# Kernel tuning notes

Hardware: AMD Instinct MI355X
Metric: run time of the kernel (lower is better)

Reference implementation:

```python
import jax, jax.numpy as jnp
import numpy as np

B, C, D, H, W = 1, 64, 24, 24, 24
N = D * H * W
K = D + H + W - 2  # cross neighbors per node (self deduped)
DS, GD = 64, 64    # d_sim, g_dim
GROUPS = C // 4
EPS = 1e-5
N_ITERS = 2        # pool_strides = [1, 1]


def _build_nbr_idx():
    i, j, k = np.meshgrid(np.arange(D), np.arange(H), np.arange(W), indexing='ij')
    i, j, k = i.reshape(-1), j.reshape(-1), k.reshape(-1)
    a0 = (j * W + k)[:, None] + np.arange(D)[None, :] * (H * W)      # (N, D) full depth line (incl self)
    full1 = (i * H * W + k)[:, None] + np.arange(H)[None, :] * W     # (N, H)
    a1 = full1[np.arange(H)[None, :] != j[:, None]].reshape(N, H - 1)
    full2 = (i * H * W + j * W)[:, None] + np.arange(W)[None, :]     # (N, W)
    a2 = full2[np.arange(W)[None, :] != k[:, None]].reshape(N, W - 1)
    return np.concatenate([a0, a1, a2], axis=1).astype(np.int32)     # (N, K)


def setup_inputs() -> dict:
    key = jax.random.key(0)
    ks = jax.random.split(key, 8)
    s = 0.05
    return {
        'x': jax.random.normal(ks[0], (B, C, D, H, W), jnp.float32),
        'nbr_idx': jnp.asarray(_build_nbr_idx()),
        'phi_w': jax.random.normal(ks[1], (DS, C), jnp.float32) * s,
        'phi_b': jnp.zeros((DS,), jnp.float32),
        'theta_w': jax.random.normal(ks[2], (DS, C), jnp.float32) * s,
        'theta_b': jnp.zeros((DS,), jnp.float32),
        'G_w': jax.random.normal(ks[3], (GD, C), jnp.float32) * s,
        'G_b': jnp.zeros((GD,), jnp.float32),
        'r_w': jax.random.normal(ks[4], (C, GD), jnp.float32) * s,
        'r_b': jnp.zeros((C,), jnp.float32),
        'gn_gamma': jnp.ones((N_ITERS, C), jnp.float32),
        'gn_beta': jnp.zeros((N_ITERS, C), jnp.float32),
        'bn_gamma': jnp.ones((C,), jnp.float32),
        'bn_beta': jnp.zeros((C,), jnp.float32),
        'bn_mean': jnp.zeros((C,), jnp.float32),
        'bn_var': jnp.ones((C,), jnp.float32),
    }


def _group_norm(v, gamma, beta):
    vg = v.reshape(B, GROUPS, C // GROUPS, D, H, W)
    m = vg.mean(axis=(2, 3, 4, 5), keepdims=True)
    var = ((vg - m) ** 2).mean(axis=(2, 3, 4, 5), keepdims=True)
    vn = ((vg - m) / jnp.sqrt(var + EPS)).reshape(B, C, D, H, W)
    return vn * gamma[None, :, None, None, None] + beta[None, :, None, None, None]


def reference(x, nbr_idx, phi_w, phi_b, theta_w, theta_b, G_w, G_b, r_w, r_b,
              gn_gamma, gn_beta, bn_gamma, bn_beta, bn_mean, bn_var):
    h = x
    for it in range(N_ITERS):
        hf = h.reshape(B, C, N).transpose(2, 0, 1)                    # (N, B, C) node features
        theta = jnp.einsum('nbc,dc->nbd', hf, theta_w) + theta_b     # (N, B, DS) queries
        phi_all = jnp.einsum('nbc,dc->nbd', hf, phi_w) + phi_b       # (N, B, DS) keys (pre-gather)
        g_all = jnp.einsum('nbc,gc->nbg', hf, G_w) + G_b             # (N, B, GD) values (pre-gather)
        phi_e = phi_all[nbr_idx]                                      # (N, K, B, DS) mailbox gather
        g_e = g_all[nbr_idx]                                          # (N, K, B, GD)
        f = jnp.einsum('nbd,nkbd->nbk', theta, phi_e)                # attention logits over K
        a = jax.nn.softmax(f, axis=-1)                                # non_local_merge 'softmax'
        y = jnp.einsum('nbk,nkbg->nbg', a, g_e)                      # weighted value sum
        cross = jnp.einsum('nbg,cg->nbc', y, r_w) + r_b              # (N, B, C) output proj
        cross = cross.transpose(1, 2, 0).reshape(B, C, D, H, W)
        h = h + _group_norm(cross, gn_gamma[it], gn_beta[it])
    # BatchNorm3d (eval, running stats) + ReLU
    bc = lambda v: v[None, :, None, None, None]
    out = (h - bc(bn_mean)) / jnp.sqrt(bc(bn_var) + EPS) * bc(bn_gamma) + bc(bn_beta)
    return jax.nn.relu(out)
```

## Files before the change

kernel.cpp:

```cpp
#include <hip/hip_runtime.h>
#include <math.h>

#define NN 13824
#define LW 24

__global__ __launch_bounds__(256) void apply_proj_kernel(
    const float* __restrict__ x,
    const float* __restrict__ cross, const float* __restrict__ gsum,
    const float* __restrict__ gn_g, const float* __restrict__ gn_b,
    float* __restrict__ h_out, int mode,
    const float* __restrict__ theta_w, const float* __restrict__ theta_b,
    const float* __restrict__ phi_w, const float* __restrict__ phi_b,
    const float* __restrict__ g_w, const float* __restrict__ g_b,
    float* __restrict__ theta, float* __restrict__ phi, float* __restrict__ gv)
{
    __shared__ float hs[64 * 64];
    __shared__ float ws[64 * 68];

    const int tid = threadIdx.x;
    const int tile = blockIdx.x / 3, ts = blockIdx.x % 3;
    const int n0 = tile * 64;

    const float* wsel = (ts == 0) ? theta_w : (ts == 1) ? phi_w : g_w;
    const float* bsel = (ts == 0) ? theta_b : (ts == 1) ? phi_b : g_b;
    float*       osel = (ts == 0) ? theta   : (ts == 1) ? phi   : gv;

    if (mode == 0) {
        for (int i = tid; i < 4096; i += 256) {
            int c = i >> 6, nl = i & 63;
            hs[c * 64 + nl] = x[(size_t)c * NN + n0 + nl];
        }
    } else {
        for (int i = tid; i < 4096; i += 256) {
            int nl = i >> 6, c = i & 63;
            ws[c * 68 + nl] = cross[(size_t)(n0 + nl) * 64 + c];
        }
        __syncthreads();
        const float inv_cnt = 1.f / 55296.f;
        for (int i = tid; i < 4096; i += 256) {
            int c = i >> 6, nl = i & 63;
            int gr = c >> 2;
            float mean = gsum[gr * 16] * inv_cnt;
            float var = gsum[512 + gr * 16] * inv_cnt - mean * mean;
            float v = (ws[c * 68 + nl] - mean) * rsqrtf(var + 1e-5f) * gn_g[c] + gn_b[c];
            size_t o = (size_t)c * NN + n0 + nl;
            float hv = x[o] + v;
            hs[c * 64 + nl] = hv;
            if (ts == 0) h_out[o] = hv;
        }
        __syncthreads();
    }

    for (int i = tid; i < 4096; i += 256) {
        int d = i >> 6, c = i & 63;
        ws[c * 68 + d] = wsel[d * 64 + c];
    }
    __syncthreads();

    const int d0  = (tid & 15) * 4;
    const int nl0 = (tid >> 4) * 4;
    float acc[4][4];
    #pragma unroll
    for (int q = 0; q < 4; q++)
        #pragma unroll
        for (int j = 0; j < 4; j++) acc[q][j] = 0.f;

    #pragma unroll 4
    for (int c = 0; c < 64; c++) {
        float4 hv = *(const float4*)&hs[c * 64 + nl0];
        float4 wv = *(const float4*)&ws[c * 68 + d0];
        #pragma unroll
        for (int j = 0; j < 4; j++) {
            float w = (&wv.x)[j];
            acc[0][j] += hv.x * w;
            acc[1][j] += hv.y * w;
            acc[2][j] += hv.z * w;
            acc[3][j] += hv.w * w;
        }
    }
    float4 bias = *(const float4*)&bsel[d0];
    #pragma unroll
    for (int q = 0; q < 4; q++) {
        float4 v;
        v.x = acc[q][0] + bias.x; v.y = acc[q][1] + bias.y;
        v.z = acc[q][2] + bias.z; v.w = acc[q][3] + bias.w;
        *(float4*)&osel[(size_t)(n0 + nl0 + q) * 64 + d0] = v;
    }
}

__global__ __launch_bounds__(128) void line_attn_kernel(
    const float* __restrict__ theta,
    const float* __restrict__ phi,
    const float* __restrict__ gv,
    float* __restrict__ y_part,
    float* __restrict__ l_part,
    float* __restrict__ gsum)
{
    __shared__ float th[2][LW * 68], ph[2][LW * 68], gs[2][LW * 68];
    __shared__ float P[2][LW * 28];

    const int tid = threadIdx.x;
    const int wv = tid >> 6, lane = tid & 63;
    const int gl = blockIdx.x * 2 + wv;
    const int axis = gl / 576, L = gl % 576;

    if (blockIdx.x == 0) {
        for (int i = tid; i < 1024; i += 128) gsum[i] = 0.f;
    }

    int base, stride;
    if (axis == 0)      { base = L * 24;                    stride = 1;   }
    else if (axis == 1) { base = (L / 24) * 576 + (L % 24); stride = 24;  }
    else                { base = L;                         stride = 576; }
    const bool excl = (axis != 2);

    #pragma unroll
    for (int q = 0; q < 6; q++) {
        int idx = q * 64 + lane;
        int row = idx >> 4, c4 = (idx & 15) * 4;
        size_t g = (size_t)(base + row * stride) * 64 + c4;
        int la = row * 68 + c4;
        *(float4*)&th[wv][la] = *(const float4*)&theta[g];
        *(float4*)&ph[wv][la] = *(const float4*)&phi[g];
        *(float4*)&gs[wv][la] = *(const float4*)&gv[g];
    }

    const int r0 = (lane >> 3) * 3, c0 = (lane & 7) * 3;
    float sa[3][3];
    #pragma unroll
    for (int a = 0; a < 3; a++)
        #pragma unroll
        for (int b = 0; b < 3; b++) sa[a][b] = 0.f;

    #pragma unroll 4
    for (int d4 = 0; d4 < 64; d4 += 4) {
        float4 t[3], p[3];
        #pragma unroll
        for (int a = 0; a < 3; a++) t[a] = *(const float4*)&th[wv][(r0 + a) * 68 + d4];
        #pragma unroll
        for (int b = 0; b < 3; b++) p[b] = *(const float4*)&ph[wv][(c0 + b) * 68 + d4];
        #pragma unroll
        for (int a = 0; a < 3; a++)
            #pragma unroll
            for (int b = 0; b < 3; b++)
                sa[a][b] += t[a].x * p[b].x + t[a].y * p[b].y +
                            t[a].z * p[b].z + t[a].w * p[b].w;
    }
    #pragma unroll
    for (int a = 0; a < 3; a++)
        #pragma unroll
        for (int b = 0; b < 3; b++) {
            float e = (excl && (r0 + a) == (c0 + b)) ? 0.f : __expf(sa[a][b]);
            P[wv][(r0 + a) * 28 + c0 + b] = e;
        }

    if (lane < 24) {
        float s = 0.f;
        #pragma unroll
        for (int c4 = 0; c4 < 24; c4 += 4) {
            float4 pv = *(const float4*)&P[wv][lane * 28 + c4];
            s += pv.x + pv.y + pv.z + pv.w;
        }
        l_part[(size_t)axis * NN + base + lane * stride] = s;
    }

    float acc[24];
    #pragma unroll
    for (int r = 0; r < 24; r++) acc[r] = 0.f;
    #pragma unroll
    for (int c4 = 0; c4 < 24; c4 += 4) {
        float g0 = gs[wv][(c4 + 0) * 68 + lane];
        float g1 = gs[wv][(c4 + 1) * 68 + lane];
        float g2 = gs[wv][(c4 + 2) * 68 + lane];
        float g3 = gs[wv][(c4 + 3) * 68 + lane];
        #pragma unroll
        for (int r = 0; r < 24; r++) {
            float4 pv = *(const float4*)&P[wv][r * 28 + c4];
            acc[r] += pv.x * g0 + pv.y * g1 + pv.z * g2 + pv.w * g3;
        }
    }
    float* yp = y_part + (size_t)axis * NN * 64;
    #pragma unroll
    for (int r = 0; r < 24; r++)
        yp[(size_t)(base + r * stride) * 64 + lane] = acc[r];
}

__global__ __launch_bounds__(256) void combine_kernel(
    const float* __restrict__ y_part, const float* __restrict__ l_part,
    const float* __restrict__ r_w, const float* __restrict__ r_b,
    float* __restrict__ cross, float* __restrict__ gsum)
{
    __shared__ float ys[16 * 68];
    __shared__ float red_s[4][64], red_ss[4][64];

    const int tid = threadIdx.x;
    const int d = tid & 63, w = tid >> 6;
    const int n0 = blockIdx.x * 16;
    const size_t S = (size_t)NN * 64;

    #pragma unroll
    for (int q = 0; q < 4; q++) {
        int nn = w * 4 + q;
        int n = n0 + nn;
        float lv = l_part[n] + l_part[NN + n] + l_part[2 * NN + n];
        size_t o = (size_t)n * 64 + d;
        float yv = y_part[o] + y_part[S + o] + y_part[2 * S + o];
        ys[nn * 68 + d] = yv / lv;
    }
    __syncthreads();

    const int c = d;
    float rb = r_b[c];
    float acc[4] = {rb, rb, rb, rb};
    for (int dd = 0; dd < 64; dd += 4) {
        float4 r4 = *(const float4*)&r_w[c * 64 + dd];
        #pragma unroll
        for (int q = 0; q < 4; q++) {
            float4 y4 = *(const float4*)&ys[(w * 4 + q) * 68 + dd];
            acc[q] += r4.x * y4.x + r4.y * y4.y + r4.z * y4.z + r4.w * y4.w;
        }
    }
    float s = 0.f, ss = 0.f;
    #pragma unroll
    for (int q = 0; q < 4; q++) {
        int n = n0 + w * 4 + q;
        cross[(size_t)n * 64 + c] = acc[q];
        s += acc[q];
        ss += acc[q] * acc[q];
    }
    red_s[w][c] = s;
    red_ss[w][c] = ss;
    __syncthreads();
    if (w == 0) {
        float ts  = red_s[0][c] + red_s[1][c] + red_s[2][c] + red_s[3][c];
        float tss = red_ss[0][c] + red_ss[1][c] + red_ss[2][c] + red_ss[3][c];
        ts  += __shfl_xor(ts, 1);  ts  += __shfl_xor(ts, 2);
        tss += __shfl_xor(tss, 1); tss += __shfl_xor(tss, 2);
        if ((c & 3) == 0) {
            atomicAdd(&gsum[(c >> 2) * 16], ts);
            atomicAdd(&gsum[512 + (c >> 2) * 16], tss);
        }
    }
}

__global__ __launch_bounds__(256) void final_kernel(
    const float* __restrict__ cross,
    const float* __restrict__ gsum,
    const float* __restrict__ gn_g, const float* __restrict__ gn_b,
    const float* __restrict__ h_in,
    const float* __restrict__ bn_g, const float* __restrict__ bn_b,
    const float* __restrict__ bn_m, const float* __restrict__ bn_v,
    float* __restrict__ out)
{
    __shared__ float t[64 * 65];
    const int tid = threadIdx.x;
    const int n0 = blockIdx.x * 64;
    for (int i = tid; i < 4096; i += 256) {
        int nl = i >> 6, c = i & 63;
        t[c * 65 + nl] = cross[(size_t)(n0 + nl) * 64 + c];
    }
    __syncthreads();
    const float inv_cnt = 1.f / 55296.f;
    for (int i = tid; i < 4096; i += 256) {
        int c = i >> 6, nl = i & 63;
        int gr = c >> 2;
        float mean = gsum[gr * 16] * inv_cnt;
        float var = gsum[512 + gr * 16] * inv_cnt - mean * mean;
        float v = (t[c * 65 + nl] - mean) * rsqrtf(var + 1e-5f) * gn_g[c] + gn_b[c];
        size_t o = (size_t)c * NN + n0 + nl;
        float h2 = h_in[o] + v;
        float bnv = (h2 - bn_m[c]) * rsqrtf(bn_v[c] + 1e-5f) * bn_g[c] + bn_b[c];
        out[o] = fmaxf(bnv, 0.f);
    }
}

extern "C" void kernel_launch(void* const* d_in, const int* in_sizes, int n_in,
                              void* d_out, int out_size, void* d_ws, size_t ws_size,
                              hipStream_t stream)
{
    const float* x        = (const float*)d_in[0];
    const float* phi_w    = (const float*)d_in[2];
    const float* phi_b    = (const float*)d_in[3];
    const float* theta_w  = (const float*)d_in[4];
    const float* theta_b  = (const float*)d_in[5];
    const float* G_w      = (const float*)d_in[6];
    const float* G_b      = (const float*)d_in[7];
    const float* r_w      = (const float*)d_in[8];
    const float* r_b      = (const float*)d_in[9];
    const float* gn_gamma = (const float*)d_in[10];
    const float* gn_beta  = (const float*)d_in[11];
    const float* bn_gamma = (const float*)d_in[12];
    const float* bn_beta  = (const float*)d_in[13];
    const float* bn_mean  = (const float*)d_in[14];
    const float* bn_var   = (const float*)d_in[15];

    float* ws = (float*)d_ws;
    const size_t S = (size_t)NN * 64;
    float* h1    = ws;
    float* theta = ws + S;
    float* phi   = ws + 2 * S;
    float* gv    = ws + 3 * S;
    float* ypart = ws + 4 * S;
    float* cross = ws + 7 * S;
    float* lpart = ws + 8 * S;
    float* gsum  = ws + 8 * S + 3 * NN;

    apply_proj_kernel<<<648, 256, 0, stream>>>(x, cross, gsum, gn_gamma, gn_beta,
                                               h1, 0,
                                               theta_w, theta_b, phi_w, phi_b,
                                               G_w, G_b, theta, phi, gv);
    line_attn_kernel<<<864, 128, 0, stream>>>(theta, phi, gv, ypart, lpart, gsum);
    combine_kernel<<<864, 256, 0, stream>>>(ypart, lpart, r_w, r_b, cross, gsum);
    apply_proj_kernel<<<648, 256, 0, stream>>>(x, cross, gsum, gn_gamma, gn_beta,
                                               h1, 1,
                                               theta_w, theta_b, phi_w, phi_b,
                                               G_w, G_b, theta, phi, gv);
    line_attn_kernel<<<864, 128, 0, stream>>>(theta, phi, gv, ypart, lpart, gsum);
    combine_kernel<<<864, 256, 0, stream>>>(ypart, lpart, r_w, r_b, cross, gsum);
    final_kernel<<<216, 256, 0, stream>>>(cross, gsum, gn_gamma + 64, gn_beta + 64,
                                          h1, bn_gamma, bn_beta, bn_mean, bn_var,
                                          (float*)d_out);
}
```

Baseline: 223.9 us.

## Interleave theta/phi/g projections and restructure line attention to read directly from global

Projection outputs are stored interleaved per node (theta, phi, g in one 192-float row), so each line fetches contiguous data. The line-attention kernel now reads theta/phi straight from global/L1 instead of staging them in LDS, prefetches g into registers, and computes row sums with wave shuffles. The P·g product is retiled into a 6x4 register block per lane with float4 stores, and blocks go from 2 to 4 waves. The aim is less LDS traffic and footprint, more resident waves, and fewer scattered loads. The risk is redundant global loads of theta/phi rows across lanes, and reliance on __threadfence_block rather than a barrier for the per-wave LDS handoff.

```diff
diff --git a/kernel.cpp b/kernel.cpp
--- a/kernel.cpp
+++ b/kernel.cpp
@@ -12,7 +12,7 @@
     const float* __restrict__ theta_w, const float* __restrict__ theta_b,
     const float* __restrict__ phi_w, const float* __restrict__ phi_b,
     const float* __restrict__ g_w, const float* __restrict__ g_b,
-    float* __restrict__ theta, float* __restrict__ phi, float* __restrict__ gv)
+    float* __restrict__ tpg)
 {
     __shared__ float hs[64 * 64];
     __shared__ float ws[64 * 68];
@@ -23,7 +23,6 @@
 
     const float* wsel = (ts == 0) ? theta_w : (ts == 1) ? phi_w : g_w;
     const float* bsel = (ts == 0) ? theta_b : (ts == 1) ? phi_b : g_b;
-    float*       osel = (ts == 0) ? theta   : (ts == 1) ? phi   : gv;
 
     if (mode == 0) {
         for (int i = tid; i < 4096; i += 256) {
@@ -84,28 +83,27 @@
         float4 v;
         v.x = acc[q][0] + bias.x; v.y = acc[q][1] + bias.y;
         v.z = acc[q][2] + bias.z; v.w = acc[q][3] + bias.w;
-        *(float4*)&osel[(size_t)(n0 + nl0 + q) * 64 + d0] = v;
-    }
-}
-
-__global__ __launch_bounds__(128) void line_attn_kernel(
-    const float* __restrict__ theta,
-    const float* __restrict__ phi,
-    const float* __restrict__ gv,
+        *(float4*)&tpg[(size_t)(n0 + nl0 + q) * 192 + ts * 64 + d0] = v;
+    }
+}
+
+__global__ __launch_bounds__(256, 4) void line_attn_kernel(
+    const float* __restrict__ tpg,
     float* __restrict__ y_part,
     float* __restrict__ l_part,
     float* __restrict__ gsum)
 {
-    __shared__ float th[2][LW * 68], ph[2][LW * 68], gs[2][LW * 68];
-    __shared__ float P[2][LW * 28];
+    __shared__ float wbuf[4][2304];
 
     const int tid = threadIdx.x;
     const int wv = tid >> 6, lane = tid & 63;
-    const int gl = blockIdx.x * 2 + wv;
-    const int axis = gl / 576, L = gl % 576;
+    const int line = blockIdx.x * 4 + wv;
+    const int axis = line / 576, L = line % 576;
+    float* gb = wbuf[wv];
+    float* P  = wbuf[wv] + 1632;
 
     if (blockIdx.x == 0) {
-        for (int i = tid; i < 1024; i += 128) gsum[i] = 0.f;
+        for (int i = tid; i < 1024; i += 256) gsum[i] = 0.f;
     }
 
     int base, stride;
@@ -114,31 +112,35 @@
     else                { base = L;                         stride = 576; }
     const bool excl = (axis != 2);
 
+    float4 gpre[6];
+    const int grow = lane >> 4, gquad = lane & 15;
     #pragma unroll
     for (int q = 0; q < 6; q++) {
-        int idx = q * 64 + lane;
-        int row = idx >> 4, c4 = (idx & 15) * 4;
-        size_t g = (size_t)(base + row * stride) * 64 + c4;
-        int la = row * 68 + c4;
-        *(float4*)&th[wv][la] = *(const float4*)&theta[g];
-        *(float4*)&ph[wv][la] = *(const float4*)&phi[g];
-        *(float4*)&gs[wv][la] = *(const float4*)&gv[g];
-    }
-
-    const int r0 = (lane >> 3) * 3, c0 = (lane & 7) * 3;
+        int row = q * 4 + grow;
+        gpre[q] = *(const float4*)&tpg[(size_t)(base + row * stride) * 192 + 128 + gquad * 4];
+    }
+
+    const int li = lane >> 3, lj = lane & 7;
+    const int r0 = li * 3, c0 = lj * 3;
+    const float* trow[3];
+    const float* prow[3];
+    #pragma unroll
+    for (int a = 0; a < 3; a++) {
+        trow[a] = tpg + (size_t)(base + (r0 + a) * stride) * 192;
+        prow[a] = tpg + (size_t)(base + (c0 + a) * stride) * 192 + 64;
+    }
     float sa[3][3];
     #pragma unroll
     for (int a = 0; a < 3; a++)
         #pragma unroll
         for (int b = 0; b < 3; b++) sa[a][b] = 0.f;
-
     #pragma unroll 4
     for (int d4 = 0; d4 < 64; d4 += 4) {
         float4 t[3], p[3];
         #pragma unroll
-        for (int a = 0; a < 3; a++) t[a] = *(const float4*)&th[wv][(r0 + a) * 68 + d4];
-        #pragma unroll
-        for (int b = 0; b < 3; b++) p[b] = *(const float4*)&ph[wv][(c0 + b) * 68 + d4];
+        for (int a = 0; a < 3; a++) t[a] = *(const float4*)&trow[a][d4];
+        #pragma unroll
+        for (int b = 0; b < 3; b++) p[b] = *(const float4*)&prow[b][d4];
         #pragma unroll
         for (int a = 0; a < 3; a++)
             #pragma unroll
@@ -146,43 +148,53 @@
                 sa[a][b] += t[a].x * p[b].x + t[a].y * p[b].y +
                             t[a].z * p[b].z + t[a].w * p[b].w;
     }
+
+    float rs[3] = {0.f, 0.f, 0.f};
     #pragma unroll
     for (int a = 0; a < 3; a++)
         #pragma unroll
         for (int b = 0; b < 3; b++) {
             float e = (excl && (r0 + a) == (c0 + b)) ? 0.f : __expf(sa[a][b]);
-            P[wv][(r0 + a) * 28 + c0 + b] = e;
-        }
-
-    if (lane < 24) {
-        float s = 0.f;
-        #pragma unroll
-        for (int c4 = 0; c4 < 24; c4 += 4) {
-            float4 pv = *(const float4*)&P[wv][lane * 28 + c4];
-            s += pv.x + pv.y + pv.z + pv.w;
-        }
-        l_part[(size_t)axis * NN + base + lane * stride] = s;
-    }
-
-    float acc[24];
-    #pragma unroll
-    for (int r = 0; r < 24; r++) acc[r] = 0.f;
-    #pragma unroll
-    for (int c4 = 0; c4 < 24; c4 += 4) {
-        float g0 = gs[wv][(c4 + 0) * 68 + lane];
-        float g1 = gs[wv][(c4 + 1) * 68 + lane];
-        float g2 = gs[wv][(c4 + 2) * 68 + lane];
-        float g3 = gs[wv][(c4 + 3) * 68 + lane];
-        #pragma unroll
-        for (int r = 0; r < 24; r++) {
-            float4 pv = *(const float4*)&P[wv][r * 28 + c4];
-            acc[r] += pv.x * g0 + pv.y * g1 + pv.z * g2 + pv.w * g3;
+            rs[a] += e;
+            P[(r0 + a) * 28 + c0 + b] = e;
+        }
+    #pragma unroll
+    for (int off = 1; off <= 4; off <<= 1)
+        #pragma unroll
+        for (int a = 0; a < 3; a++) rs[a] += __shfl_xor(rs[a], off);
+    if (lj == 0) {
+        #pragma unroll
+        for (int a = 0; a < 3; a++)
+            l_part[(size_t)axis * NN + base + (r0 + a) * stride] = rs[a];
+    }
+
+    #pragma unroll
+    for (int q = 0; q < 6; q++)
+        *(float4*)&gb[(q * 4 + grow) * 68 + gquad * 4] = gpre[q];
+    __threadfence_block();
+
+    const int rg = lane >> 4, dg = lane & 15;
+    float acc[6][4];
+    #pragma unroll
+    for (int i = 0; i < 6; i++)
+        #pragma unroll
+        for (int k = 0; k < 4; k++) acc[i][k] = 0.f;
+    #pragma unroll 4
+    for (int c = 0; c < 24; c++) {
+        float4 gv = *(const float4*)&gb[c * 68 + dg * 4];
+        #pragma unroll
+        for (int i = 0; i < 6; i++) {
+            float p = P[(rg * 6 + i) * 28 + c];
+            acc[i][0] += p * gv.x; acc[i][1] += p * gv.y;
+            acc[i][2] += p * gv.z; acc[i][3] += p * gv.w;
         }
     }
     float* yp = y_part + (size_t)axis * NN * 64;
     #pragma unroll
-    for (int r = 0; r < 24; r++)
-        yp[(size_t)(base + r * stride) * 64 + lane] = acc[r];
+    for (int i = 0; i < 6; i++) {
+        float4 v = {acc[i][0], acc[i][1], acc[i][2], acc[i][3]};
+        *(float4*)&yp[(size_t)(base + (rg * 6 + i) * stride) * 64 + dg * 4] = v;
+    }
 }
 
 __global__ __launch_bounds__(256) void combine_kernel(
@@ -297,9 +309,7 @@
     float* ws = (float*)d_ws;
     const size_t S = (size_t)NN * 64;
     float* h1    = ws;
-    float* theta = ws + S;
-    float* phi   = ws + 2 * S;
-    float* gv    = ws + 3 * S;
+    float* tpg   = ws + S;
     float* ypart = ws + 4 * S;
     float* cross = ws + 7 * S;
     float* lpart = ws + 8 * S;
@@ -308,14 +318,14 @@
     apply_proj_kernel<<<648, 256, 0, stream>>>(x, cross, gsum, gn_gamma, gn_beta,
                                                h1, 0,
                                                theta_w, theta_b, phi_w, phi_b,
-                                               G_w, G_b, theta, phi, gv);
-    line_attn_kernel<<<864, 128, 0, stream>>>(theta, phi, gv, ypart, lpart, gsum);
+                                               G_w, G_b, tpg);
+    line_attn_kernel<<<432, 256, 0, stream>>>(tpg, ypart, lpart, gsum);
     combine_kernel<<<864, 256, 0, stream>>>(ypart, lpart, r_w, r_b, cross, gsum);
     apply_proj_kernel<<<648, 256, 0, stream>>>(x, cross, gsum, gn_gamma, gn_beta,
                                                h1, 1,
                                                theta_w, theta_b, phi_w, phi_b,
-                                               G_w, G_b, theta, phi, gv);
-    line_attn_kernel<<<864, 128, 0, stream>>>(theta, phi, gv, ypart, lpart, gsum);
+                                               G_w, G_b, tpg);
+    line_attn_kernel<<<432, 256, 0, stream>>>(tpg, ypart, lpart, gsum);
     combine_kernel<<<864, 256, 0, stream>>>(ypart, lpart, r_w, r_b, cross, gsum);
     final_kernel<<<216, 256, 0, stream>>>(cross, gsum, gn_gamma + 64, gn_beta + 64,
                                           h1, bn_gamma, bn_beta, bn_mean, bn_var,
```

Result: slower. 233.0 us (+4.0%).
